# Performance work log

Hardware: AMD Instinct MI355X
Metric: run time of the kernel (lower is better)

## Reference

```python
import jax, jax.numpy as jnp
import numpy as np

DIM = 1024
MLP_MULT = 4
NUM_EXPERTS = 8
EXPERT_HIDDEN = MLP_MULT * DIM // NUM_EXPERTS  # 512


def setup_inputs() -> dict:
    key = jax.random.key(0)
    k_x, k_r, k_fc, k_pj = jax.random.split(key, 4)
    x = jax.random.normal(k_x, (4, 4096, DIM), dtype=jnp.float32)
    # router: nn.Linear(dim, num_experts, bias=False) -> weight [E, D]
    w_router = jax.random.normal(k_r, (NUM_EXPERTS, DIM), dtype=jnp.float32) * (1.0 / np.sqrt(DIM))
    # per-expert fc: Linear(dim, hidden) weight [H, D]; stacked [E, H, D]
    w_fc = jax.random.normal(k_fc, (NUM_EXPERTS, EXPERT_HIDDEN, DIM), dtype=jnp.float32) * (1.0 / np.sqrt(DIM))
    # per-expert proj: Linear(hidden, dim) weight [D, H]; stacked [E, D, H]
    # (_zero_init in the original; use small random values so the reference output is non-trivial)
    w_proj = jax.random.normal(k_pj, (NUM_EXPERTS, DIM, EXPERT_HIDDEN), dtype=jnp.float32) * (1.0 / np.sqrt(EXPERT_HIDDEN))
    return {"x": x, "w_router": w_router, "w_fc": w_fc, "w_proj": w_proj}


def reference(x, w_router, w_fc, w_proj):
    # Router on detached input; top-1 expert per token.
    logits = jnp.einsum('bsd,ed->bse', jax.lax.stop_gradient(x), w_router)
    weights = jax.nn.softmax(logits, axis=-1)  # computed as in original (unused in output)
    indices = jnp.argmax(weights, axis=-1)     # [B, S]
    onehot = jax.nn.one_hot(indices, NUM_EXPERTS, dtype=x.dtype)  # [B, S, E]
    # Dense dispatch: run all experts, combine with one-hot (equivalent to mask gather/scatter).
    h = jnp.einsum('bsd,ehd->bseh', x, w_fc)              # [B, S, E, H]
    h = jnp.where(h >= 0, h, 0.5 * h)                      # leaky_relu(negative_slope=0.5)
    h = h * h                                              # square
    out = jnp.einsum('bseh,edh,bse->bsd', h, w_proj, onehot)
    return out
```

## Files before the change

kernel.cpp:

```cpp
#include <hip/hip_runtime.h>
#include <stdint.h>
#include <stddef.h>

#define DIM 1024
#define NEXP 8
#define HID 512
#define NTOK 16384
#define NB_HIST 64

typedef __attribute__((ext_vector_type(4))) float f32x4;
typedef __attribute__((ext_vector_type(8))) short short8;
typedef __attribute__((ext_vector_type(4))) unsigned short u16x4;

__device__ __forceinline__ unsigned short f2b(float f) {
  unsigned int u = __float_as_uint(f);
  return (unsigned short)((u + 0x7FFFu + ((u >> 16) & 1u)) >> 16);
}

__device__ __forceinline__ void gload_lds16(const unsigned short* g, unsigned short* l) {
  __builtin_amdgcn_global_load_lds((const __attribute__((address_space(1))) void*)g,
                                   (__attribute__((address_space(3))) void*)l, 16, 0, 0);
}

__global__ __launch_bounds__(256) void k_router(const float* __restrict__ x,
                                                const float* __restrict__ wr,
                                                int* __restrict__ eid,
                                                unsigned short* __restrict__ xb) {
  int wid = threadIdx.x >> 6, lane = threadIdx.x & 63;
  int tok = blockIdx.x * 4 + wid;
  const float* xr = x + (size_t)tok * DIM;
  unsigned short* xbr = xb + (size_t)tok * DIM;
  float s[NEXP];
#pragma unroll
  for (int e = 0; e < NEXP; e++) s[e] = 0.f;
#pragma unroll
  for (int i = 0; i < 4; i++) {
    f32x4 xv = *(const f32x4*)(xr + lane * 4 + 256 * i);
    u16x4 u;
    u.x = f2b(xv.x); u.y = f2b(xv.y); u.z = f2b(xv.z); u.w = f2b(xv.w);
    *(u16x4*)(xbr + lane * 4 + 256 * i) = u;
#pragma unroll
    for (int e = 0; e < NEXP; e++) {
      f32x4 wv = *(const f32x4*)(wr + e * DIM + lane * 4 + 256 * i);
      s[e] += xv.x * wv.x + xv.y * wv.y + xv.z * wv.z + xv.w * wv.w;
    }
  }
#pragma unroll
  for (int e = 0; e < NEXP; e++) {
    float v = s[e];
#pragma unroll
    for (int off = 32; off > 0; off >>= 1) v += __shfl_xor(v, off);
    s[e] = v;
  }
  if (lane == 0) {
    int be = 0;
    float bv = s[0];
#pragma unroll
    for (int e = 1; e < NEXP; e++) {
      if (s[e] > bv) { bv = s[e]; be = e; }
    }
    eid[tok] = be;
  }
}

__global__ __launch_bounds__(256) void k_hist(const int* __restrict__ eid,
                                              int* __restrict__ bc) {
  __shared__ int h[NEXP];
  if (threadIdx.x < NEXP) h[threadIdx.x] = 0;
  __syncthreads();
  int tok = blockIdx.x * (NTOK / NB_HIST) + threadIdx.x;
  atomicAdd(&h[eid[tok]], 1);
  __syncthreads();
  if (threadIdx.x < NEXP) bc[blockIdx.x * NEXP + threadIdx.x] = h[threadIdx.x];
}

__global__ void k_scan(const int* __restrict__ bc, int* __restrict__ offs,
                       int* __restrict__ base) {
  __shared__ int cnt[NEXP];
  __shared__ int so[NEXP + 1];
  int t = threadIdx.x;
  if (t < NEXP) {
    int run = 0;
    for (int b = 0; b < NB_HIST; b++) {
      base[b * NEXP + t] = run;
      run += bc[b * NEXP + t];
    }
    cnt[t] = run;
  }
  __syncthreads();
  if (t == 0) {
    int a = 0;
    for (int e = 0; e < NEXP; e++) { so[e] = a; a += cnt[e]; }
    so[NEXP] = a;
  }
  __syncthreads();
  if (t < NEXP + 1) offs[t] = so[t];
  for (int i = t; i < NB_HIST * NEXP; i += blockDim.x) base[i] += so[i % NEXP];
}

__global__ __launch_bounds__(256) void k_scatter(const int* __restrict__ eid,
                                                 const int* __restrict__ base,
                                                 int* __restrict__ tlist) {
  __shared__ int cur[NEXP];
  if (threadIdx.x < NEXP) cur[threadIdx.x] = base[blockIdx.x * NEXP + threadIdx.x];
  __syncthreads();
  int tok = blockIdx.x * (NTOK / NB_HIST) + threadIdx.x;
  int e = eid[tok];
  int pos = atomicAdd(&cur[e], 1);
  tlist[pos] = tok;
}

__global__ __launch_bounds__(256) void k_cast(const float* __restrict__ a,
                                              const float* __restrict__ b,
                                              unsigned short* __restrict__ oa,
                                              unsigned short* __restrict__ ob) {
  const int n4 = NEXP * HID * DIM / 4;
  int stride = gridDim.x * blockDim.x;
  for (int i = blockIdx.x * blockDim.x + threadIdx.x; i < n4; i += stride) {
    f32x4 va = ((const f32x4*)a)[i];
    f32x4 vb = ((const f32x4*)b)[i];
    u16x4 ua, ub;
    ua.x = f2b(va.x); ua.y = f2b(va.y); ua.z = f2b(va.z); ua.w = f2b(va.w);
    ub.x = f2b(vb.x); ub.y = f2b(vb.y); ub.z = f2b(vb.z); ub.w = f2b(vb.w);
    ((u16x4*)oa)[i] = ua;
    ((u16x4*)ob)[i] = ub;
  }
}

template <int KDIM, int NDIM, int NB, bool IS_FC>
__global__ __launch_bounds__(256) void k_gemm(
    const unsigned short* __restrict__ xb, const unsigned short* __restrict__ hin,
    const unsigned short* __restrict__ wb, const int* __restrict__ offs,
    const int* __restrict__ tlist, unsigned short* __restrict__ hout,
    float* __restrict__ out) {
  int l = ((int)blockIdx.x & 7) * ((int)gridDim.x >> 3) + ((int)blockIdx.x >> 3);
  int e = -1, mb = 0, nb = 0, acc2 = 0;
#pragma unroll
  for (int i = 0; i < NEXP; i++) {
    int mi = offs[i + 1] - offs[i];
    int tb = ((mi + 127) >> 7) * NB;
    if (e < 0 && l < acc2 + tb) {
      int r = l - acc2;
      e = i; mb = r / NB; nb = r % NB;
    }
    acc2 += tb;
  }
  if (e < 0) return;
  int off = offs[e];
  int me = offs[e + 1] - off;
  int m0 = mb * 128;
  int n0 = nb * 128;

  __shared__ unsigned short As[2][128 * 64];
  __shared__ unsigned short Bs[2][128 * 64];

  int t = threadIdx.x;
  int lane = t & 63, w = t >> 6;
  int wm = w >> 1, wn = w & 1;

  int srow = w * 8 + (lane >> 3);
  int kb = (lane & 7) ^ ((lane >> 3) & 7);

  const unsigned short* asrc[4];
  const unsigned short* bsrc[4];
#pragma unroll
  for (int i = 0; i < 4; i++) {
    int r = i * 32 + srow;
    int gm = m0 + r;
    if (gm > me - 1) gm = me - 1;
    if (IS_FC) {
      int tok = tlist[off + gm];
      asrc[i] = xb + (size_t)tok * KDIM + kb * 8;
    } else {
      asrc[i] = hin + (size_t)(off + gm) * KDIM + kb * 8;
    }
    bsrc[i] = wb + ((size_t)e * NDIM + n0 + r) * (size_t)KDIM + kb * 8;
  }

  f32x4 acc[4][4] = {};
  const int NT = KDIM / 64;

#pragma unroll
  for (int i = 0; i < 4; i++) {
    gload_lds16(asrc[i], &As[0][i * 2048 + w * 512]);
    gload_lds16(bsrc[i], &Bs[0][i * 2048 + w * 512]);
  }

  for (int kt = 0; kt < NT; kt++) {
    int cur = kt & 1;
    if (kt + 1 < NT) {
#pragma unroll
      for (int i = 0; i < 4; i++) {
        gload_lds16(asrc[i] + (kt + 1) * 64, &As[cur ^ 1][i * 2048 + w * 512]);
        gload_lds16(bsrc[i] + (kt + 1) * 64, &Bs[cur ^ 1][i * 2048 + w * 512]);
      }
      asm volatile("s_waitcnt vmcnt(8)" ::: "memory");
    } else {
      asm volatile("s_waitcnt vmcnt(0)" ::: "memory");
    }
    __builtin_amdgcn_s_barrier();

    const unsigned short* Ac = As[cur];
    const unsigned short* Bc = Bs[cur];
#pragma unroll
    for (int ks = 0; ks < 2; ks++) {
      short8 af[4], bf[4];
#pragma unroll
      for (int i = 0; i < 4; i++) {
        int ra = wm * 64 + i * 16 + (lane & 15);
        int ca = (ks * 4 + (lane >> 4)) ^ (ra & 7);
        af[i] = *(const short8*)&Ac[ra * 64 + ca * 8];
        int rb = wn * 64 + i * 16 + (lane & 15);
        int cb = (ks * 4 + (lane >> 4)) ^ (rb & 7);
        bf[i] = *(const short8*)&Bc[rb * 64 + cb * 8];
      }
      __builtin_amdgcn_s_setprio(1);
#pragma unroll
      for (int mi = 0; mi < 4; mi++)
#pragma unroll
        for (int ni = 0; ni < 4; ni++)
          acc[mi][ni] =
              __builtin_amdgcn_mfma_f32_16x16x32_bf16(af[mi], bf[ni], acc[mi][ni], 0, 0, 0);
      __builtin_amdgcn_s_setprio(0);
    }
    __builtin_amdgcn_s_barrier();
  }

  int rb = (lane >> 4) * 4, cb = lane & 15;
#pragma unroll
  for (int mi = 0; mi < 4; mi++) {
#pragma unroll
    for (int j = 0; j < 4; j++) {
      int ml = wm * 64 + mi * 16 + rb + j;
      if (m0 + ml < me) {
        if (IS_FC) {
#pragma unroll
          for (int ni = 0; ni < 4; ni++) {
            int col = n0 + wn * 64 + ni * 16 + cb;
            float v = acc[mi][ni][j];
            v = (v >= 0.f) ? v * v : 0.25f * v * v;
            hout[(size_t)(off + m0 + ml) * HID + col] = f2b(v);
          }
        } else {
          int tok = tlist[off + m0 + ml];
#pragma unroll
          for (int ni = 0; ni < 4; ni++) {
            int col = n0 + wn * 64 + ni * 16 + cb;
            out[(size_t)tok * DIM + col] = acc[mi][ni][j];
          }
        }
      }
    }
  }
}

extern "C" void kernel_launch(void* const* d_in, const int* in_sizes, int n_in,
                              void* d_out, int out_size, void* d_ws, size_t ws_size,
                              hipStream_t stream) {
  const float* x = (const float*)d_in[0];
  const float* wr = (const float*)d_in[1];
  const float* wfc = (const float*)d_in[2];
  const float* wpj = (const float*)d_in[3];
  float* out = (float*)d_out;

  uintptr_t p = (uintptr_t)d_ws;
  int* offs = (int*)p;  p += 256;
  int* bc = (int*)p;    p += sizeof(int) * NB_HIST * NEXP;
  int* base = (int*)p;  p += sizeof(int) * NB_HIST * NEXP;
  int* eid = (int*)p;   p += sizeof(int) * NTOK;
  int* tlist = (int*)p; p += sizeof(int) * NTOK;
  unsigned short* wfc_b = (unsigned short*)p; p += (size_t)NEXP * HID * DIM * 2;
  unsigned short* wpj_b = (unsigned short*)p; p += (size_t)NEXP * DIM * HID * 2;
  unsigned short* hbuf = (unsigned short*)p;  p += (size_t)NTOK * HID * 2;
  unsigned short* xb = (unsigned short*)p;    p += (size_t)NTOK * DIM * 2;

  k_router<<<NTOK / 4, 256, 0, stream>>>(x, wr, eid, xb);
  k_cast<<<1024, 256, 0, stream>>>(wfc, wpj, wfc_b, wpj_b);
  k_hist<<<NB_HIST, 256, 0, stream>>>(eid, bc);
  k_scan<<<1, 256, 0, stream>>>(bc, offs, base);
  k_scatter<<<NB_HIST, 256, 0, stream>>>(eid, base, tlist);
  k_gemm<1024, 512, 4, true><<<dim3(544), 256, 0, stream>>>(
      xb, nullptr, wfc_b, offs, tlist, hbuf, nullptr);
  k_gemm<512, 1024, 8, false><<<dim3(1080), 256, 0, stream>>>(
      nullptr, hbuf, wpj_b, offs, tlist, nullptr, out);
}
```

Baseline: 119.6 us.

## Switch grouped MoE GEMM to three-stage LDS pipeline with K-tile of 32

Replaces the double-buffered 64-wide K tiles with a triple-buffered ring of 32-wide K tiles. Loads run two tiles ahead, and only one barrier is issued per iteration instead of two. The aim is better overlap of global-to-LDS loads with MFMA work and less barrier stall. In exchange, each barrier covers half as much compute, there are twice as many iterations, and the swizzle on 32-wide rows may raise LDS bank conflicts.

```diff
diff --git a/kernel.cpp b/kernel.cpp
--- a/kernel.cpp
+++ b/kernel.cpp
@@ -151,21 +151,19 @@
   int m0 = mb * 128;
   int n0 = nb * 128;
 
-  __shared__ unsigned short As[2][128 * 64];
-  __shared__ unsigned short Bs[2][128 * 64];
+  __shared__ unsigned short lds[3][2][128 * 32];
 
   int t = threadIdx.x;
   int lane = t & 63, w = t >> 6;
   int wm = w >> 1, wn = w & 1;
 
-  int srow = w * 8 + (lane >> 3);
-  int kb = (lane & 7) ^ ((lane >> 3) & 7);
-
-  const unsigned short* asrc[4];
-  const unsigned short* bsrc[4];
-#pragma unroll
-  for (int i = 0; i < 4; i++) {
-    int r = i * 32 + srow;
+  int kb = (lane & 3) ^ ((lane >> 2) & 3);
+
+  const unsigned short* asrc[2];
+  const unsigned short* bsrc[2];
+#pragma unroll
+  for (int i = 0; i < 2; i++) {
+    int r = i * 64 + w * 16 + (lane >> 2);
     int gm = m0 + r;
     if (gm > me - 1) gm = me - 1;
     if (IS_FC) {
@@ -178,53 +176,56 @@
   }
 
   f32x4 acc[4][4] = {};
-  const int NT = KDIM / 64;
-
-#pragma unroll
-  for (int i = 0; i < 4; i++) {
-    gload_lds16(asrc[i], &As[0][i * 2048 + w * 512]);
-    gload_lds16(bsrc[i], &Bs[0][i * 2048 + w * 512]);
-  }
+  const int NT = KDIM / 32;
+
+  unsigned short* b0a = &lds[0][0][0]; unsigned short* b0b = &lds[0][1][0];
+  unsigned short* b1a = &lds[1][0][0]; unsigned short* b1b = &lds[1][1][0];
+  unsigned short* b2a = &lds[2][0][0]; unsigned short* b2b = &lds[2][1][0];
+
+#define STAGE(kt_, da_, db_)                                   \
+  do {                                                         \
+    gload_lds16(asrc[0] + (kt_) * 32, (da_) + (w * 16) * 32);  \
+    gload_lds16(asrc[1] + (kt_) * 32, (da_) + (64 + w * 16) * 32); \
+    gload_lds16(bsrc[0] + (kt_) * 32, (db_) + (w * 16) * 32);  \
+    gload_lds16(bsrc[1] + (kt_) * 32, (db_) + (64 + w * 16) * 32); \
+  } while (0)
+
+  STAGE(0, b0a, b0b);
+  STAGE(1, b1a, b1b);
 
   for (int kt = 0; kt < NT; kt++) {
-    int cur = kt & 1;
-    if (kt + 1 < NT) {
-#pragma unroll
-      for (int i = 0; i < 4; i++) {
-        gload_lds16(asrc[i] + (kt + 1) * 64, &As[cur ^ 1][i * 2048 + w * 512]);
-        gload_lds16(bsrc[i] + (kt + 1) * 64, &Bs[cur ^ 1][i * 2048 + w * 512]);
-      }
-      asm volatile("s_waitcnt vmcnt(8)" ::: "memory");
+    if (kt < NT - 1) {
+      asm volatile("s_waitcnt vmcnt(4)" ::: "memory");
     } else {
       asm volatile("s_waitcnt vmcnt(0)" ::: "memory");
     }
     __builtin_amdgcn_s_barrier();
 
-    const unsigned short* Ac = As[cur];
-    const unsigned short* Bc = Bs[cur];
-#pragma unroll
-    for (int ks = 0; ks < 2; ks++) {
-      short8 af[4], bf[4];
-#pragma unroll
-      for (int i = 0; i < 4; i++) {
-        int ra = wm * 64 + i * 16 + (lane & 15);
-        int ca = (ks * 4 + (lane >> 4)) ^ (ra & 7);
-        af[i] = *(const short8*)&Ac[ra * 64 + ca * 8];
-        int rb = wn * 64 + i * 16 + (lane & 15);
-        int cb = (ks * 4 + (lane >> 4)) ^ (rb & 7);
-        bf[i] = *(const short8*)&Bc[rb * 64 + cb * 8];
-      }
-      __builtin_amdgcn_s_setprio(1);
-#pragma unroll
-      for (int mi = 0; mi < 4; mi++)
-#pragma unroll
-        for (int ni = 0; ni < 4; ni++)
-          acc[mi][ni] =
-              __builtin_amdgcn_mfma_f32_16x16x32_bf16(af[mi], bf[ni], acc[mi][ni], 0, 0, 0);
-      __builtin_amdgcn_s_setprio(0);
-    }
-    __builtin_amdgcn_s_barrier();
-  }
+    if (kt + 2 < NT) STAGE(kt + 2, b2a, b2b);
+
+    short8 af[4], bf[4];
+#pragma unroll
+    for (int i = 0; i < 4; i++) {
+      int ra = wm * 64 + i * 16 + (lane & 15);
+      int ca = (lane >> 4) ^ (ra & 3);
+      af[i] = *(const short8*)&b0a[ra * 32 + ca * 8];
+      int rb = wn * 64 + i * 16 + (lane & 15);
+      int cb = (lane >> 4) ^ (rb & 3);
+      bf[i] = *(const short8*)&b0b[rb * 32 + cb * 8];
+    }
+    __builtin_amdgcn_s_setprio(1);
+#pragma unroll
+    for (int mi = 0; mi < 4; mi++)
+#pragma unroll
+      for (int ni = 0; ni < 4; ni++)
+        acc[mi][ni] =
+            __builtin_amdgcn_mfma_f32_16x16x32_bf16(af[mi], bf[ni], acc[mi][ni], 0, 0, 0);
+    __builtin_amdgcn_s_setprio(0);
+
+    unsigned short* ta = b0a; b0a = b1a; b1a = b2a; b2a = ta;
+    unsigned short* tb = b0b; b0b = b1b; b1b = b2b; b2b = tb;
+  }
+#undef STAGE
 
   int rb = (lane >> 4) * 4, cb = lane & 15;
 #pragma unroll
```

Result: faster. 112.6 us (-5.8%).
